# Performance work log

Measured on AMD Instinct MI355X. Metric: run time of the kernel, lower is better.

Reference implementation:

```python
import jax, jax.numpy as jnp
import numpy as np

B, C, H, W = 8, 192, 48, 48
D_EXP = 384   # d_expand = 2*d_model
D_INNER = 384 # min(ssm_rank_ratio, ssm_ratio)*d_model == d_expand -> no low-rank
K = 4         # scan directions
N = 16        # d_state
R = 12        # dt_rank = ceil(192/16)


def setup_inputs() -> dict:
    key = jax.random.key(0)
    ks = jax.random.split(key, 9)
    return {
        "x": jax.random.normal(ks[0], (B, C, H, W), jnp.float32),
        "in_proj_w": jax.random.normal(ks[1], (2 * D_EXP, C), jnp.float32) * 0.02,
        "conv_w": jax.random.normal(ks[2], (D_EXP, 1, 3, 3), jnp.float32) * 0.1,
        "conv_b": jax.random.normal(ks[3], (D_EXP,), jnp.float32) * 0.02,
        "x_proj_w": jax.random.normal(ks[4], (K, R + 2 * N, D_INNER), jnp.float32) * 0.05,
        "dt_w": jax.random.normal(ks[5], (K, D_INNER, R), jnp.float32) * 0.1,
        "dt_b": jax.random.normal(ks[6], (K, D_INNER), jnp.float32) * 0.1,
        "A_logs": jax.random.uniform(ks[7], (K * D_INNER, N), jnp.float32, -1.0, 1.0),
        "Ds": jnp.ones((K * D_INNER,), jnp.float32),
        "ln_w": jnp.ones((D_INNER,), jnp.float32),
        "ln_b": jnp.zeros((D_INNER,), jnp.float32),
        "out_proj_w": jax.random.normal(ks[8], (C, D_EXP), jnp.float32) * 0.02,
    }


def selective_scan(u, delta, A, Bs, Cs, Dskip):
    # u, delta: (B,K,D,L); A: (K,D,N); Bs, Cs: (B,K,N,L); Dskip: (K,D)
    uT = u.transpose(3, 0, 1, 2)       # (L,B,K,D)
    dT = delta.transpose(3, 0, 1, 2)
    BT = Bs.transpose(3, 0, 1, 2)      # (L,B,K,N)
    CT = Cs.transpose(3, 0, 1, 2)
    h0 = jnp.zeros((u.shape[0], K, u.shape[2], A.shape[-1]), u.dtype)  # (B,K,D,N)

    def step(h, xs_t):
        d_t, u_t, B_t, C_t = xs_t
        dA = jnp.exp(d_t[..., None] * A)                              # (B,K,D,N)
        h = h * dA + (d_t * u_t)[..., None] * B_t[:, :, None, :]      # discretized B*u
        y = jnp.einsum('bkdn,bkn->bkd', h, C_t)
        return h, y

    _, ys = jax.lax.scan(step, h0, (dT, uT, BT, CT))  # ys: (L,B,K,D)
    ys = ys.transpose(1, 2, 3, 0)                     # (B,K,D,L)
    return ys + u * Dskip[None, :, :, None]


def reference(x, in_proj_w, conv_w, conv_b, x_proj_w, dt_w, dt_b, A_logs, Ds, ln_w, ln_b, out_proj_w):
    # in_proj 1x1 conv (no bias), then chunk into (x, z)
    xz = jnp.einsum('bchw,oc->bohw', x, in_proj_w)
    xx, z = jnp.split(xz, 2, axis=1)
    z1 = jax.nn.gelu(z, approximate=False)  # nn.GELU() is exact erf form
    # depthwise 3x3 conv, padding=1
    xx = jax.lax.conv_general_dilated(
        xx, conv_w, (1, 1), 'SAME', feature_group_count=D_EXP,
        dimension_numbers=('NCHW', 'OIHW', 'NCHW')) + conv_b[None, :, None, None]
    xx = jax.nn.gelu(xx, approximate=False)

    Bb, Dd, Hh, Ww = xx.shape
    L = Hh * Ww
    # CrossScan: 4 traversal orders
    x_hw = xx.reshape(Bb, Dd, L)
    x_wh = xx.transpose(0, 1, 3, 2).reshape(Bb, Dd, L)
    xs = jnp.stack([x_hw, x_wh, x_hw[..., ::-1], x_wh[..., ::-1]], axis=1)  # (B,4,D,L)

    x_dbl = jnp.einsum('bkdl,kcd->bkcl', xs, x_proj_w)
    dts, Bs_, Cs_ = jnp.split(x_dbl, [R, R + N], axis=2)  # (B,K,R,L),(B,K,N,L),(B,K,N,L)
    dts = jnp.einsum('bkrl,kdr->bkdl', dts, dt_w)
    delta = jax.nn.softplus(dts + dt_b[None, :, :, None])
    A = -jnp.exp(A_logs).reshape(K, D_INNER, N)

    ys = selective_scan(xs, delta, A, Bs_, Cs_, Ds.reshape(K, D_INNER))  # (B,4,D,L)

    # CrossMerge: unflip reversed dirs, untranspose dir 1, sum
    ys = ys[:, 0:2] + ys[:, 2:4, :, ::-1]
    y = ys[:, 0] + ys[:, 1].reshape(Bb, Dd, Ww, Hh).transpose(0, 1, 3, 2).reshape(Bb, Dd, L)

    # out_norm LayerNorm over channel, v0 shape: (B,L,D)
    y = y.transpose(0, 2, 1)
    mu = y.mean(-1, keepdims=True)
    var = ((y - mu) ** 2).mean(-1, keepdims=True)
    y = (y - mu) / jnp.sqrt(var + 1e-5) * ln_w + ln_b
    y = y.reshape(Bb, Hh, Ww, Dd).transpose(0, 3, 1, 2)  # (B,D,H,W)

    y = y * z1
    out = jnp.einsum('bdhw,cd->bchw', y, out_proj_w)
    return out
```

## Files before the change

kernel.cpp:

```cpp
#include <hip/hip_runtime.h>
#include <cstdint>


static constexpr int L = 2304;

typedef __attribute__((ext_vector_type(8))) short short8;
typedef __attribute__((ext_vector_type(8))) unsigned short ushort8;
typedef __attribute__((ext_vector_type(4))) float f32x4;

__device__ __forceinline__ float gelu_f(float x) {
  return 0.5f * x * (1.0f + erff(x * 0.70710678118654752440f));
}

__device__ __forceinline__ unsigned short bf16r(float f) {
  unsigned u = __float_as_uint(f);
  u += 0x7FFF + ((u >> 16) & 1);
  return (unsigned short)(u >> 16);
}

__global__ __launch_bounds__(256) void k_inproj(const float* __restrict__ x,
                                                const float* __restrict__ Wp,
                                                float* __restrict__ xx,
                                                float* __restrict__ z1T) {
  const int b = blockIdx.z;
  const int m0 = blockIdx.y * 64;
  const int n0 = blockIdx.x * 64;
  const int tid = threadIdx.x;
  const int lane = tid & 63, wv = tid >> 6;
  const int ln = lane & 15, qd = lane >> 4;
  __shared__ unsigned short Abf[64][40];
  __shared__ unsigned short Bbf[64][40];
  __shared__ float zt[64][68];
  f32x4 acc[4] = {};
  const float* xb = x + (size_t)b * 192 * L;
  for (int c0 = 0; c0 < 192; c0 += 32) {
    {
      const int row = tid >> 2, kk = (tid & 3) * 8;
      float4 a0 = *(const float4*)&Wp[(size_t)(m0 + row) * 192 + c0 + kk];
      float4 a1 = *(const float4*)&Wp[(size_t)(m0 + row) * 192 + c0 + kk + 4];
      ushort8 v = {bf16r(a0.x), bf16r(a0.y), bf16r(a0.z), bf16r(a0.w),
                   bf16r(a1.x), bf16r(a1.y), bf16r(a1.z), bf16r(a1.w)};
      *(ushort8*)&Abf[row][kk] = v;
    }
    {
      const int kr = tid >> 3, nc = tid & 7;
      const float* src = &xb[(size_t)(c0 + kr) * L + n0 + nc * 8];
      float4 b0 = *(const float4*)&src[0];
      float4 b1 = *(const float4*)&src[4];
      Bbf[nc * 8 + 0][kr] = bf16r(b0.x);
      Bbf[nc * 8 + 1][kr] = bf16r(b0.y);
      Bbf[nc * 8 + 2][kr] = bf16r(b0.z);
      Bbf[nc * 8 + 3][kr] = bf16r(b0.w);
      Bbf[nc * 8 + 4][kr] = bf16r(b1.x);
      Bbf[nc * 8 + 5][kr] = bf16r(b1.y);
      Bbf[nc * 8 + 6][kr] = bf16r(b1.z);
      Bbf[nc * 8 + 7][kr] = bf16r(b1.w);
    }
    __syncthreads();
    short8 af = *(short8*)&Abf[16 * wv + ln][8 * qd];
#pragma unroll
    for (int j = 0; j < 4; ++j) {
      short8 bf = *(short8*)&Bbf[16 * j + ln][8 * qd];
      acc[j] = __builtin_amdgcn_mfma_f32_16x16x32_bf16(af, bf, acc[j], 0, 0, 0);
    }
    __syncthreads();
  }
  if (m0 < 384) {
    float* xxb = xx + ((size_t)b * 384 + m0 + 16 * wv + 4 * qd) * L + n0 + ln;
#pragma unroll
    for (int j = 0; j < 4; ++j)
#pragma unroll
      for (int r = 0; r < 4; ++r) xxb[(size_t)r * L + 16 * j] = acc[j][r];
  } else {
#pragma unroll
    for (int j = 0; j < 4; ++j)
#pragma unroll
      for (int r = 0; r < 4; ++r)
        zt[16 * j + ln][16 * wv + 4 * qd + r] = gelu_f(acc[j][r]);
    __syncthreads();
    const int r = tid >> 2, cb = (tid & 3) * 16;
#pragma unroll
    for (int q = 0; q < 4; ++q) {
      int c = cb + q * 4;
      float4 v = make_float4(zt[r][c], zt[r][c + 1], zt[r][c + 2], zt[r][c + 3]);
      *(float4*)&z1T[((size_t)b * L + n0 + r) * 384 + (m0 - 384) + c] = v;
    }
  }
}

__global__ __launch_bounds__(256) void k_conv(const float* __restrict__ xx,
                                              const float* __restrict__ conv_w,
                                              const float* __restrict__ conv_b,
                                              float* __restrict__ xc,
                                              float* __restrict__ xcT) {
  const int bid = blockIdx.x;
  const int d = bid % 384, b = bid / 384;
  const int tid = threadIdx.x;
  __shared__ float ls[48 * 49];
  __shared__ float xg[48 * 49];
  const float* src = xx + ((size_t)b * 384 + d) * L;
  for (int i = tid; i < L; i += 256) ls[(i / 48) * 49 + (i % 48)] = src[i];
  float cw[9];
  const float* cwp = conv_w + (size_t)d * 9;
#pragma unroll
  for (int r = 0; r < 9; ++r) cw[r] = cwp[r];
  const float cb = conv_b[d];
  __syncthreads();
  float* dst = xc + ((size_t)b * 384 + d) * L;
  for (int p = tid; p < L; p += 256) {
    int h = p / 48, w = p % 48;
    float acc = cb;
#pragma unroll
    for (int dy = -1; dy <= 1; ++dy) {
      int hh = h + dy;
      if (hh < 0 || hh >= 48) continue;
#pragma unroll
      for (int dx = -1; dx <= 1; ++dx) {
        int ww = w + dx;
        if (ww < 0 || ww >= 48) continue;
        acc = fmaf(ls[hh * 49 + ww], cw[(dy + 1) * 3 + (dx + 1)], acc);
      }
    }
    float g = gelu_f(acc);
    dst[p] = g;
    xg[h * 49 + w] = g;
  }
  __syncthreads();
  float* dstT = xcT + ((size_t)b * 384 + d) * L;
  for (int j = tid; j < L; j += 256) {
    int h = j % 48, w = j / 48;
    dstT[j] = xg[h * 49 + w];
  }
}

__global__ __launch_bounds__(256) void k_xdbl(const float* __restrict__ xc,
                                              const float* __restrict__ xcT,
                                              const float* __restrict__ xpw,
                                              float* __restrict__ xdbl) {
  const int n0 = blockIdx.x * 64;
  const int bk = blockIdx.y;
  const int b = bk >> 2, k = bk & 3;
  const int tid = threadIdx.x;
  const int lane = tid & 63, wv = tid >> 6;
  const int ln = lane & 15, qd = lane >> 4;
  __shared__ unsigned short Abf[64][40];
  __shared__ unsigned short Bbf[64][40];
  f32x4 acc[4] = {};
  const float* src = ((k & 1) ? xcT : xc) + (size_t)b * 384 * L;
  const bool rev = (k >= 2);
  const float* ap = xpw + (size_t)k * 44 * 384;
  for (int c0 = 0; c0 < 384; c0 += 32) {
    {
      const int row = tid >> 2, kk = (tid & 3) * 8;
      ushort8 v = {0, 0, 0, 0, 0, 0, 0, 0};
      if (row < 44) {
        float4 a0 = *(const float4*)&ap[(size_t)row * 384 + c0 + kk];
        float4 a1 = *(const float4*)&ap[(size_t)row * 384 + c0 + kk + 4];
        v = ushort8{bf16r(a0.x), bf16r(a0.y), bf16r(a0.z), bf16r(a0.w),
                    bf16r(a1.x), bf16r(a1.y), bf16r(a1.z), bf16r(a1.w)};
      }
      *(ushort8*)&Abf[row][kk] = v;
    }
    {
      const int kr = tid >> 3, nc = tid & 7;
      const float* sr = src + (size_t)(c0 + kr) * L;
      const int base = n0 + nc * 8;
      float vals[8];
      if (!rev) {
        float4 f0 = *(const float4*)&sr[base];
        float4 f1 = *(const float4*)&sr[base + 4];
        vals[0] = f0.x; vals[1] = f0.y; vals[2] = f0.z; vals[3] = f0.w;
        vals[4] = f1.x; vals[5] = f1.y; vals[6] = f1.z; vals[7] = f1.w;
      } else {
        float4 f0 = *(const float4*)&sr[2300 - base];
        float4 f1 = *(const float4*)&sr[2296 - base];
        vals[0] = f0.w; vals[1] = f0.z; vals[2] = f0.y; vals[3] = f0.x;
        vals[4] = f1.w; vals[5] = f1.z; vals[6] = f1.y; vals[7] = f1.x;
      }
      Bbf[nc * 8 + 0][kr] = bf16r(vals[0]);
      Bbf[nc * 8 + 1][kr] = bf16r(vals[1]);
      Bbf[nc * 8 + 2][kr] = bf16r(vals[2]);
      Bbf[nc * 8 + 3][kr] = bf16r(vals[3]);
      Bbf[nc * 8 + 4][kr] = bf16r(vals[4]);
      Bbf[nc * 8 + 5][kr] = bf16r(vals[5]);
      Bbf[nc * 8 + 6][kr] = bf16r(vals[6]);
      Bbf[nc * 8 + 7][kr] = bf16r(vals[7]);
    }
    __syncthreads();
    short8 af = *(short8*)&Abf[16 * wv + ln][8 * qd];
#pragma unroll
    for (int j = 0; j < 4; ++j) {
      short8 bf = *(short8*)&Bbf[16 * j + ln][8 * qd];
      acc[j] = __builtin_amdgcn_mfma_f32_16x16x32_bf16(af, bf, acc[j], 0, 0, 0);
    }
    __syncthreads();
  }
  const int mbase = 16 * wv + 4 * qd;
  float* ob = xdbl + ((size_t)bk * 48 + mbase) * L + n0 + ln;
#pragma unroll
  for (int r = 0; r < 4; ++r) {
    if (mbase + r < 44) {
#pragma unroll
      for (int j = 0; j < 4; ++j) ob[(size_t)r * L + 16 * j] = acc[j][r];
    }
  }
}

__global__ __launch_bounds__(256) void k_transp(const float* __restrict__ xc,
                                                float* __restrict__ uT) {
  const int l0 = blockIdx.x * 64;
  const int d0 = blockIdx.y * 64;
  const int b = blockIdx.z;
  const int tid = threadIdx.x;
  __shared__ float ls[64][65];
  const float* src = xc + (size_t)b * 384 * L;
#pragma unroll
  for (int p = 0; p < 16; ++p) {
    int i = tid + p * 256;
    int row = i >> 6, col = i & 63;
    ls[row][col] = src[(size_t)(d0 + row) * L + l0 + col];
  }
  __syncthreads();
  float* dst = uT + (size_t)b * L * 384;
#pragma unroll
  for (int p = 0; p < 16; ++p) {
    int i = tid + p * 256;
    int lrow = i >> 6, dcol = i & 63;
    dst[(size_t)(l0 + lrow) * 384 + d0 + dcol] = ls[dcol][lrow];
  }
}

__global__ __launch_bounds__(256, 4) void k_scan(const float* __restrict__ xc,
                                                 const float* __restrict__ xcT,
                                                 const float* __restrict__ xdbl,
                                                 const float* __restrict__ dt_w,
                                                 const float* __restrict__ dt_b,
                                                 const float* __restrict__ A_logs,
                                                 float* __restrict__ ys) {
  const int bid = blockIdx.x;
  const int dth = bid % 3;
  const int c = (bid / 3) % 9;
  const int k = (bid / 27) % 4;
  const int b = bid / 108;
  const int tid = threadIdx.x;
  const int dloc = tid >> 1;
  const int nh = tid & 1;
  const int d = dth * 128 + dloc;
  const int kd = k * 384 + d;
  const bool rev = (k >= 2);

  float a2[8], h[8];
#pragma unroll
  for (int n = 0; n < 8; ++n) {
    a2[n] = -__builtin_amdgcn_exp2f(A_logs[(size_t)kd * 16 + 8 * nh + n] *
                                    1.44269504088896f) *
            1.44269504088896f;
    h[n] = 0.0f;
  }
  float dtw[12];
#pragma unroll
  for (int r = 0; r < 12; ++r) dtw[r] = dt_w[(size_t)kd * 12 + r];
  const float dtb = dt_b[kd];
  const float* xd = xdbl + (size_t)(b * 4 + k) * 48 * L;
  const float* urow = ((k & 1) ? xcT : xc) + ((size_t)b * 384 + d) * L;
  float* ysb = ys + (size_t)(b * 4 + k) * L * 384 + d;

  __shared__ __align__(16) float dtrT[32][20];
  __shared__ __align__(16) float BT[32][20];
  __shared__ __align__(16) float CT[32][20];
  __shared__ __align__(16) float dds[32][258];

  const int t_own = c * 256;
  const int t_first = (c == 0) ? 0 : t_own - 128;
  const int nwin = (c == 0) ? 8 : 12;

  for (int w = 0; w < nwin; ++w) {
    const int t0 = t_first + w * 32;
    __syncthreads();
#pragma unroll
    for (int it = 0; it < 6; ++it) {
      int idx = tid + it * 256;
      if (idx < 1408) {
        int r = idx >> 5, t = idx & 31;
        float v = xd[(size_t)r * L + t0 + t];
        if (r < 12) dtrT[t][r] = v;
        else if (r < 28) BT[t][r - 12] = v;
        else CT[t][r - 28] = v;
      }
    }
    __syncthreads();
    {
      const int tl0 = nh * 16;
#pragma unroll
      for (int q = 0; q < 4; ++q) {
        const int tg = t0 + tl0 + 4 * q;
        float4 u4;
        if (!rev) {
          u4 = *(const float4*)&urow[tg];
        } else {
          float4 tmp = *(const float4*)&urow[2300 - tg];
          u4 = make_float4(tmp.w, tmp.z, tmp.y, tmp.x);
        }
        float uv[4] = {u4.x, u4.y, u4.z, u4.w};
#pragma unroll
        for (int j = 0; j < 4; ++j) {
          const int tl = tl0 + 4 * q + j;
          float4 r0 = *(const float4*)&dtrT[tl][0];
          float4 r1 = *(const float4*)&dtrT[tl][4];
          float4 r2 = *(const float4*)&dtrT[tl][8];
          float raw = dtb;
          raw = fmaf(dtw[0], r0.x, raw);
          raw = fmaf(dtw[1], r0.y, raw);
          raw = fmaf(dtw[2], r0.z, raw);
          raw = fmaf(dtw[3], r0.w, raw);
          raw = fmaf(dtw[4], r1.x, raw);
          raw = fmaf(dtw[5], r1.y, raw);
          raw = fmaf(dtw[6], r1.z, raw);
          raw = fmaf(dtw[7], r1.w, raw);
          raw = fmaf(dtw[8], r2.x, raw);
          raw = fmaf(dtw[9], r2.y, raw);
          raw = fmaf(dtw[10], r2.z, raw);
          raw = fmaf(dtw[11], r2.w, raw);
          float E = __builtin_amdgcn_exp2f(raw * 1.44269504088896f);
          float sp = (raw > 20.0f)
                         ? raw
                         : 0.69314718055994531f * __builtin_amdgcn_logf(1.0f + E);
          *(float2*)&dds[tl][2 * dloc] = make_float2(sp, sp * uv[j]);
        }
      }
    }
    __syncthreads();
    if (t0 >= t_own) {
#pragma unroll 4
      for (int s = 0; s < 32; ++s) {
        float2 p = *(const float2*)&dds[s][2 * dloc];
        float4 B0 = *(const float4*)&BT[s][8 * nh];
        float4 B1 = *(const float4*)&BT[s][8 * nh + 4];
        float4 C0 = *(const float4*)&CT[s][8 * nh];
        float4 C1 = *(const float4*)&CT[s][8 * nh + 4];
        float e0 = __builtin_amdgcn_exp2f(p.x * a2[0]);
        float e1 = __builtin_amdgcn_exp2f(p.x * a2[1]);
        float e2 = __builtin_amdgcn_exp2f(p.x * a2[2]);
        float e3 = __builtin_amdgcn_exp2f(p.x * a2[3]);
        float e4 = __builtin_amdgcn_exp2f(p.x * a2[4]);
        float e5 = __builtin_amdgcn_exp2f(p.x * a2[5]);
        float e6 = __builtin_amdgcn_exp2f(p.x * a2[6]);
        float e7 = __builtin_amdgcn_exp2f(p.x * a2[7]);
        h[0] = fmaf(h[0], e0, p.y * B0.x);
        h[1] = fmaf(h[1], e1, p.y * B0.y);
        h[2] = fmaf(h[2], e2, p.y * B0.z);
        h[3] = fmaf(h[3], e3, p.y * B0.w);
        h[4] = fmaf(h[4], e4, p.y * B1.x);
        h[5] = fmaf(h[5], e5, p.y * B1.y);
        h[6] = fmaf(h[6], e6, p.y * B1.z);
        h[7] = fmaf(h[7], e7, p.y * B1.w);
        float y = h[0] * C0.x;
        y = fmaf(h[1], C0.y, y);
        y = fmaf(h[2], C0.z, y);
        y = fmaf(h[3], C0.w, y);
        y = fmaf(h[4], C1.x, y);
        y = fmaf(h[5], C1.y, y);
        y = fmaf(h[6], C1.z, y);
        y = fmaf(h[7], C1.w, y);
        float yo = __int_as_float(__builtin_amdgcn_update_dpp(
            0, __float_as_int(y), 0xB1, 0xF, 0xF, true));
        y += yo;
        if (nh == 0) ysb[(size_t)(t0 + s) * 384] = y;
      }
    } else {
#pragma unroll 4
      for (int s = 0; s < 32; ++s) {
        float2 p = *(const float2*)&dds[s][2 * dloc];
        float4 B0 = *(const float4*)&BT[s][8 * nh];
        float4 B1 = *(const float4*)&BT[s][8 * nh + 4];
        float e0 = __builtin_amdgcn_exp2f(p.x * a2[0]);
        float e1 = __builtin_amdgcn_exp2f(p.x * a2[1]);
        float e2 = __builtin_amdgcn_exp2f(p.x * a2[2]);
        float e3 = __builtin_amdgcn_exp2f(p.x * a2[3]);
        float e4 = __builtin_amdgcn_exp2f(p.x * a2[4]);
        float e5 = __builtin_amdgcn_exp2f(p.x * a2[5]);
        float e6 = __builtin_amdgcn_exp2f(p.x * a2[6]);
        float e7 = __builtin_amdgcn_exp2f(p.x * a2[7]);
        h[0] = fmaf(h[0], e0, p.y * B0.x);
        h[1] = fmaf(h[1], e1, p.y * B0.y);
        h[2] = fmaf(h[2], e2, p.y * B0.z);
        h[3] = fmaf(h[3], e3, p.y * B0.w);
        h[4] = fmaf(h[4], e4, p.y * B1.x);
        h[5] = fmaf(h[5], e5, p.y * B1.y);
        h[6] = fmaf(h[6], e6, p.y * B1.z);
        h[7] = fmaf(h[7], e7, p.y * B1.w);
      }
    }
  }
}

__global__ __launch_bounds__(384) void k_merge(const float* __restrict__ ys,
                                               const float* __restrict__ z1T,
                                               const float* __restrict__ uT,
                                               const float* __restrict__ Ds,
                                               const float* __restrict__ ln_w,
                                               const float* __restrict__ ln_b,
                                               float* __restrict__ yln) {
  const int b = blockIdx.x / L;
  const int l = blockIdx.x % L;
  const int d = threadIdx.x;
  const int hh = l / 48, ww = l % 48;
  const int j = ww * 48 + hh;
  const float sumD = Ds[d] + Ds[384 + d] + Ds[768 + d] + Ds[1152 + d];
  const float* base = ys + (size_t)b * 4 * L * 384;
  float v = base[(size_t)(0 * L + l) * 384 + d] +
            base[(size_t)(1 * L + j) * 384 + d] +
            base[(size_t)(2 * L + (2303 - l)) * 384 + d] +
            base[(size_t)(3 * L + (2303 - j)) * 384 + d];
  v = fmaf(uT[((size_t)b * L + l) * 384 + d], sumD, v);
  float s1 = v, s2 = v * v;
#pragma unroll
  for (int off = 32; off; off >>= 1) {
    s1 += __shfl_xor(s1, off);
    s2 += __shfl_xor(s2, off);
  }
  __shared__ float ps1[6], ps2[6];
  const int wv = threadIdx.x >> 6;
  if ((threadIdx.x & 63) == 0) { ps1[wv] = s1; ps2[wv] = s2; }
  __syncthreads();
  float t1 = 0.f, t2 = 0.f;
#pragma unroll
  for (int i = 0; i < 6; ++i) { t1 += ps1[i]; t2 += ps2[i]; }
  const float mu = t1 * (1.0f / 384.0f);
  const float var = t2 * (1.0f / 384.0f) - mu * mu;
  const float rs = rsqrtf(var + 1e-5f);
  const float yv = (v - mu) * rs * ln_w[d] + ln_b[d];
  yln[((size_t)b * L + l) * 384 + d] = yv * z1T[((size_t)b * L + l) * 384 + d];
}

__global__ __launch_bounds__(256) void k_outproj(const float* __restrict__ yln,
                                                 const float* __restrict__ W2,
                                                 float* __restrict__ out) {
  const int n0 = blockIdx.x * 64;
  const int m0 = blockIdx.y * 64;
  const int b = blockIdx.z;
  const int tid = threadIdx.x;
  const int lane = tid & 63, wv = tid >> 6;
  const int ln = lane & 15, qd = lane >> 4;
  __shared__ unsigned short Abf[64][40];
  __shared__ unsigned short Bbf[64][40];
  f32x4 acc[4] = {};
  const float* yb = yln + (size_t)b * L * 384;
  for (int k0 = 0; k0 < 384; k0 += 32) {
    const int row = tid >> 2, kk = (tid & 3) * 8;
    {
      float4 a0 = *(const float4*)&W2[(size_t)(m0 + row) * 384 + k0 + kk];
      float4 a1 = *(const float4*)&W2[(size_t)(m0 + row) * 384 + k0 + kk + 4];
      ushort8 v = {bf16r(a0.x), bf16r(a0.y), bf16r(a0.z), bf16r(a0.w),
                   bf16r(a1.x), bf16r(a1.y), bf16r(a1.z), bf16r(a1.w)};
      *(ushort8*)&Abf[row][kk] = v;
    }
    {
      float4 b0 = *(const float4*)&yb[(size_t)(n0 + row) * 384 + k0 + kk];
      float4 b1 = *(const float4*)&yb[(size_t)(n0 + row) * 384 + k0 + kk + 4];
      ushort8 v = {bf16r(b0.x), bf16r(b0.y), bf16r(b0.z), bf16r(b0.w),
                   bf16r(b1.x), bf16r(b1.y), bf16r(b1.z), bf16r(b1.w)};
      *(ushort8*)&Bbf[row][kk] = v;
    }
    __syncthreads();
    short8 af = *(short8*)&Abf[16 * wv + ln][8 * qd];
#pragma unroll
    for (int j = 0; j < 4; ++j) {
      short8 bf = *(short8*)&Bbf[16 * j + ln][8 * qd];
      acc[j] = __builtin_amdgcn_mfma_f32_16x16x32_bf16(af, bf, acc[j], 0, 0, 0);
    }
    __syncthreads();
  }
  float* ob = out + ((size_t)b * 192 + m0 + 16 * wv + 4 * qd) * L + n0 + ln;
#pragma unroll
  for (int j = 0; j < 4; ++j)
#pragma unroll
    for (int r = 0; r < 4; ++r) ob[(size_t)r * L + 16 * j] = acc[j][r];
}

extern "C" void kernel_launch(void* const* d_in, const int* in_sizes, int n_in,
                              void* d_out, int out_size, void* d_ws, size_t ws_size,
                              hipStream_t stream) {
  const float* x = (const float*)d_in[0];
  const float* in_proj_w = (const float*)d_in[1];
  const float* conv_w = (const float*)d_in[2];
  const float* conv_b = (const float*)d_in[3];
  const float* x_proj_w = (const float*)d_in[4];
  const float* dt_w = (const float*)d_in[5];
  const float* dt_b = (const float*)d_in[6];
  const float* A_logs = (const float*)d_in[7];
  const float* Ds = (const float*)d_in[8];
  const float* ln_w = (const float*)d_in[9];
  const float* ln_b = (const float*)d_in[10];
  const float* out_proj_w = (const float*)d_in[11];
  float* out = (float*)d_out;
  float* ws = (float*)d_ws;

  const size_t SZ_BDL = (size_t)8 * 384 * L;
  float* xx = ws;
  float* z1T = xx + SZ_BDL;
  float* xconv = z1T + SZ_BDL;
  float* xconvT = xconv + SZ_BDL;
  float* xdbl = xconvT + SZ_BDL;
  float* ys = xdbl + (size_t)8 * 4 * 48 * L;
  float* uT = xx;
  float* yln = xx;

  k_inproj<<<dim3(36, 12, 8), 256, 0, stream>>>(x, in_proj_w, xx, z1T);
  k_conv<<<dim3(3072), 256, 0, stream>>>(xx, conv_w, conv_b, xconv, xconvT);
  k_xdbl<<<dim3(36, 32), 256, 0, stream>>>(xconv, xconvT, x_proj_w, xdbl);
  k_transp<<<dim3(36, 6, 8), 256, 0, stream>>>(xconv, uT);
  k_scan<<<dim3(864), 256, 0, stream>>>(xconv, xconvT, xdbl, dt_w, dt_b,
                                        A_logs, ys);
  k_merge<<<dim3(8 * L), 384, 0, stream>>>(ys, z1T, uT, Ds, ln_w, ln_b, yln);
  k_outproj<<<dim3(36, 3, 8), 256, 0, stream>>>(yln, out_proj_w, out);
}
```

Before: 374.4 us.

## Split scan into more time chunks and pack delta terms as bf16 in LDS

The chunked selective scan now uses 12 chunks of 192 timesteps per (batch, direction, d-third) instead of 9 chunks of 256, raising the grid from 864 to 1152 blocks. Each non-first chunk still warms up over a 128-step overlap, so the share of redundant warm-up work rises. The per-timestep delta and delta*u values are packed as two bf16 halves in one 32-bit LDS word, halving that shared buffer and its read traffic. The bf16 rounding of delta and delta*u adds precision loss to the recurrence.

After: 413.0 us. +10.3%, slower.

```diff
diff --git a/kernel.cpp b/kernel.cpp
--- a/kernel.cpp
+++ b/kernel.cpp
@@ -239,9 +239,9 @@
                                                  float* __restrict__ ys) {
   const int bid = blockIdx.x;
   const int dth = bid % 3;
-  const int c = (bid / 3) % 9;
-  const int k = (bid / 27) % 4;
-  const int b = bid / 108;
+  const int c = (bid / 3) % 12;
+  const int k = (bid / 36) % 4;
+  const int b = bid / 144;
   const int tid = threadIdx.x;
   const int dloc = tid >> 1;
   const int nh = tid & 1;
@@ -268,11 +268,11 @@
   __shared__ __align__(16) float dtrT[32][20];
   __shared__ __align__(16) float BT[32][20];
   __shared__ __align__(16) float CT[32][20];
-  __shared__ __align__(16) float dds[32][258];
-
-  const int t_own = c * 256;
+  __shared__ unsigned int dds[32][132];
+
+  const int t_own = c * 192;
   const int t_first = (c == 0) ? 0 : t_own - 128;
-  const int nwin = (c == 0) ? 8 : 12;
+  const int nwin = (c == 0) ? 6 : 10;
 
   for (int w = 0; w < nwin; ++w) {
     const int t0 = t_first + w * 32;
@@ -325,7 +325,9 @@
           float sp = (raw > 20.0f)
                          ? raw
                          : 0.69314718055994531f * __builtin_amdgcn_logf(1.0f + E);
-          *(float2*)&dds[tl][2 * dloc] = make_float2(sp, sp * uv[j]);
+          float spu = sp * uv[j];
+          dds[tl][dloc] =
+              (unsigned)bf16r(sp) | ((unsigned)bf16r(spu) << 16);
         }
       }
     }
@@ -333,27 +335,29 @@
     if (t0 >= t_own) {
 #pragma unroll 4
       for (int s = 0; s < 32; ++s) {
-        float2 p = *(const float2*)&dds[s][2 * dloc];
+        unsigned pk = dds[s][dloc];
+        float px = __uint_as_float(pk << 16);
+        float py = __uint_as_float(pk & 0xFFFF0000u);
         float4 B0 = *(const float4*)&BT[s][8 * nh];
         float4 B1 = *(const float4*)&BT[s][8 * nh + 4];
         float4 C0 = *(const float4*)&CT[s][8 * nh];
         float4 C1 = *(const float4*)&CT[s][8 * nh + 4];
-        float e0 = __builtin_amdgcn_exp2f(p.x * a2[0]);
-        float e1 = __builtin_amdgcn_exp2f(p.x * a2[1]);
-        float e2 = __builtin_amdgcn_exp2f(p.x * a2[2]);
-        float e3 = __builtin_amdgcn_exp2f(p.x * a2[3]);
-        float e4 = __builtin_amdgcn_exp2f(p.x * a2[4]);
-        float e5 = __builtin_amdgcn_exp2f(p.x * a2[5]);
-        float e6 = __builtin_amdgcn_exp2f(p.x * a2[6]);
-        float e7 = __builtin_amdgcn_exp2f(p.x * a2[7]);
-        h[0] = fmaf(h[0], e0, p.y * B0.x);
-        h[1] = fmaf(h[1], e1, p.y * B0.y);
-        h[2] = fmaf(h[2], e2, p.y * B0.z);
-        h[3] = fmaf(h[3], e3, p.y * B0.w);
-        h[4] = fmaf(h[4], e4, p.y * B1.x);
-        h[5] = fmaf(h[5], e5, p.y * B1.y);
-        h[6] = fmaf(h[6], e6, p.y * B1.z);
-        h[7] = fmaf(h[7], e7, p.y * B1.w);
+        float e0 = __builtin_amdgcn_exp2f(px * a2[0]);
+        float e1 = __builtin_amdgcn_exp2f(px * a2[1]);
+        float e2 = __builtin_amdgcn_exp2f(px * a2[2]);
+        float e3 = __builtin_amdgcn_exp2f(px * a2[3]);
+        float e4 = __builtin_amdgcn_exp2f(px * a2[4]);
+        float e5 = __builtin_amdgcn_exp2f(px * a2[5]);
+        float e6 = __builtin_amdgcn_exp2f(px * a2[6]);
+        float e7 = __builtin_amdgcn_exp2f(px * a2[7]);
+        h[0] = fmaf(h[0], e0, py * B0.x);
+        h[1] = fmaf(h[1], e1, py * B0.y);
+        h[2] = fmaf(h[2], e2, py * B0.z);
+        h[3] = fmaf(h[3], e3, py * B0.w);
+        h[4] = fmaf(h[4], e4, py * B1.x);
+        h[5] = fmaf(h[5], e5, py * B1.y);
+        h[6] = fmaf(h[6], e6, py * B1.z);
+        h[7] = fmaf(h[7], e7, py * B1.w);
         float y = h[0] * C0.x;
         y = fmaf(h[1], C0.y, y);
         y = fmaf(h[2], C0.z, y);
@@ -370,25 +374,27 @@
     } else {
 #pragma unroll 4
       for (int s = 0; s < 32; ++s) {
-        float2 p = *(const float2*)&dds[s][2 * dloc];
+        unsigned pk = dds[s][dloc];
+        float px = __uint_as_float(pk << 16);
+        float py = __uint_as_float(pk & 0xFFFF0000u);
         float4 B0 = *(const float4*)&BT[s][8 * nh];
         float4 B1 = *(const float4*)&BT[s][8 * nh + 4];
-        float e0 = __builtin_amdgcn_exp2f(p.x * a2[0]);
-        float e1 = __builtin_amdgcn_exp2f(p.x * a2[1]);
-        float e2 = __builtin_amdgcn_exp2f(p.x * a2[2]);
-        float e3 = __builtin_amdgcn_exp2f(p.x * a2[3]);
-        float e4 = __builtin_amdgcn_exp2f(p.x * a2[4]);
-        float e5 = __builtin_amdgcn_exp2f(p.x * a2[5]);
-        float e6 = __builtin_amdgcn_exp2f(p.x * a2[6]);
-        float e7 = __builtin_amdgcn_exp2f(p.x * a2[7]);
-        h[0] = fmaf(h[0], e0, p.y * B0.x);
-        h[1] = fmaf(h[1], e1, p.y * B0.y);
-        h[2] = fmaf(h[2], e2, p.y * B0.z);
-        h[3] = fmaf(h[3], e3, p.y * B0.w);
-        h[4] = fmaf(h[4], e4, p.y * B1.x);
-        h[5] = fmaf(h[5], e5, p.y * B1.y);
-        h[6] = fmaf(h[6], e6, p.y * B1.z);
-        h[7] = fmaf(h[7], e7, p.y * B1.w);
+        float e0 = __builtin_amdgcn_exp2f(px * a2[0]);
+        float e1 = __builtin_amdgcn_exp2f(px * a2[1]);
+        float e2 = __builtin_amdgcn_exp2f(px * a2[2]);
+        float e3 = __builtin_amdgcn_exp2f(px * a2[3]);
+        float e4 = __builtin_amdgcn_exp2f(px * a2[4]);
+        float e5 = __builtin_amdgcn_exp2f(px * a2[5]);
+        float e6 = __builtin_amdgcn_exp2f(px * a2[6]);
+        float e7 = __builtin_amdgcn_exp2f(px * a2[7]);
+        h[0] = fmaf(h[0], e0, py * B0.x);
+        h[1] = fmaf(h[1], e1, py * B0.y);
+        h[2] = fmaf(h[2], e2, py * B0.z);
+        h[3] = fmaf(h[3], e3, py * B0.w);
+        h[4] = fmaf(h[4], e4, py * B1.x);
+        h[5] = fmaf(h[5], e5, py * B1.y);
+        h[6] = fmaf(h[6], e6, py * B1.z);
+        h[7] = fmaf(h[7], e7, py * B1.w);
       }
     }
   }
@@ -510,8 +516,8 @@
   k_conv<<<dim3(3072), 256, 0, stream>>>(xx, conv_w, conv_b, xconv, xconvT);
   k_xdbl<<<dim3(36, 32), 256, 0, stream>>>(xconv, xconvT, x_proj_w, xdbl);
   k_transp<<<dim3(36, 6, 8), 256, 0, stream>>>(xconv, uT);
-  k_scan<<<dim3(864), 256, 0, stream>>>(xconv, xconvT, xdbl, dt_w, dt_b,
-                                        A_logs, ys);
+  k_scan<<<dim3(1152), 256, 0, stream>>>(xconv, xconvT, xdbl, dt_w, dt_b,
+                                         A_logs, ys);
   k_merge<<<dim3(8 * L), 384, 0, stream>>>(ys, z1T, uT, Ds, ln_w, ln_b, yln);
   k_outproj<<<dim3(36, 3, 8), 256, 0, stream>>>(yln, out_proj_w, out);
 }
```
